# Optimization experiments

Measured on AMD Instinct MI355X. Metric: run time of the kernel, lower is better.

Reference implementation:

```python
import jax, jax.numpy as jnp
import numpy as np

B, S, D = 4, 2048, 1024
H = 16
HS = D // H  # 64


def setup_inputs() -> dict:
    key = jax.random.key(0)
    ks = jax.random.split(key, 6)
    scale = 1.0 / np.sqrt(D)
    x = jax.random.normal(ks[0], (B, S, D), dtype=jnp.float32)
    # per-head projection weights, stacked: [H, D, HS]
    Wq = jax.random.normal(ks[1], (H, D, HS), dtype=jnp.float32) * scale
    Wk = jax.random.normal(ks[2], (H, D, HS), dtype=jnp.float32) * scale
    Wv = jax.random.normal(ks[3], (H, D, HS), dtype=jnp.float32) * scale
    Wo = jax.random.normal(ks[4], (D, D), dtype=jnp.float32) * scale
    bo = jax.random.normal(ks[5], (D,), dtype=jnp.float32) * 0.01
    return {"x": x, "Wq": Wq, "Wk": Wk, "Wv": Wv, "Wo": Wo, "bo": bo}


def reference(x, Wq, Wk, Wv, Wo, bo):
    # Per-head dense projections (no bias): [B,S,D] x [H,D,HS] -> [B,H,S,HS]
    q = jnp.einsum('bsd,hde->bhse', x, Wq)
    k = jnp.einsum('bsd,hde->bhse', x, Wk)
    v = jnp.einsum('bsd,hde->bhse', x, Wv)
    # scaled dot-product scores: [B,H,S,S]
    scores = jnp.einsum('bhse,bhte->bhst', q, k) / jnp.sqrt(jnp.asarray(HS, dtype=x.dtype))
    # causal mask (lower triangular kept)
    causal = jnp.tril(jnp.ones((S, S), dtype=bool))
    scores = jnp.where(causal, scores, -jnp.inf)
    attn = jax.nn.softmax(scores, axis=-1)
    # dropout is identity at inference (rate handled as 0)
    out = jnp.einsum('bhst,bhte->bhse', attn, v)  # [B,H,S,HS]
    # concat heads: [B,S,H*HS] = [B,S,D]
    out = jnp.transpose(out, (0, 2, 1, 3)).reshape(B, S, D)
    return out @ Wo + bo
```

## Files before the change

### kernel.cpp

```cpp
#include <hip/hip_runtime.h>
#include <hip/hip_bf16.h>
#include <stdint.h>

#define NB 4
#define NS 2048
#define ND 1024
#define NH 16
#define NHS 64
#define NEG_BIG (-1e30f)
#define Q_SCALE 0.18033688011112042f

typedef __bf16 bf16x8 __attribute__((ext_vector_type(8)));
typedef float floatx4 __attribute__((ext_vector_type(4)));
typedef short s16x4 __attribute__((ext_vector_type(4)));

#if defined(__has_builtin)
#if __has_builtin(__builtin_amdgcn_mfma_f32_16x16x16bf16_1k)
#define HAVE_MFMA1K 1
#endif
#endif
#ifndef HAVE_MFMA1K
#define HAVE_MFMA1K 0
#endif

static constexpr size_t WSLAB = (size_t)NH * ND * NHS;
static constexpr size_t QSLAB = (size_t)NB * NH * NS * NHS;
static constexpr size_t XSLAB = (size_t)NB * NS * ND;

__device__ __forceinline__ uint16_t f2b(float f) {
    union { __hip_bfloat16 h; uint16_t u; } cv;
    cv.h = __float2bfloat16(f);
    return cv.u;
}

__device__ __forceinline__ void gll16(const void* g, void* l) {
  __builtin_amdgcn_global_load_lds(
      (__attribute__((address_space(1))) void*)(uintptr_t)g,
      (__attribute__((address_space(3))) void*)(uintptr_t)l,
      16, 0, 0);
}

__global__ __launch_bounds__(256) void k_prep(
    const float* __restrict__ x, const float* __restrict__ Wq,
    const float* __restrict__ Wk, const float* __restrict__ Wv,
    const float* __restrict__ Wo, uint16_t* __restrict__ xb,
    uint16_t* __restrict__ wt) {
  __shared__ __align__(16) uint16_t T[64][72];
  int bid = blockIdx.x;
  int tid = threadIdx.x;
  if (bid < 4096) {
    size_t i0 = ((size_t)bid * 256 + tid) * 8;
    float4 f0 = *(const float4*)&x[i0];
    float4 f1 = *(const float4*)&x[i0 + 4];
    __align__(16) uint16_t tmp[8];
    tmp[0] = f2b(f0.x); tmp[1] = f2b(f0.y); tmp[2] = f2b(f0.z); tmp[3] = f2b(f0.w);
    tmp[4] = f2b(f1.x); tmp[5] = f2b(f1.y); tmp[6] = f2b(f1.z); tmp[7] = f2b(f1.w);
    *(uint4*)&xb[i0] = *(uint4*)tmp;
    return;
  }
  bid -= 4096;
  const float* src; uint16_t* dst;
  int srcStride, dstStride, r0, c0;
  if (bid < 768) {
    int mat = bid >> 8;
    int rem = bid & 255;
    int h = rem >> 4, dt = rem & 15;
    const float* W = (mat == 0) ? Wq : (mat == 1) ? Wk : Wv;
    src = W + (size_t)h * (ND * NHS);
    dst = wt + (size_t)mat * WSLAB + (size_t)h * (NHS * ND);
    srcStride = NHS; dstStride = ND;
    r0 = dt * 64; c0 = 0;
  } else {
    int rem = bid - 768;
    int dt = rem >> 4, et = rem & 15;
    src = Wo; dst = wt + 3 * WSLAB;
    srcStride = ND; dstStride = ND;
    r0 = dt * 64; c0 = et * 64;
  }
  for (int u = tid; u < 1024; u += 256) {
    int row = u >> 4, cq = u & 15;
    float4 f = *(const float4*)&src[(size_t)(r0 + row) * srcStride + c0 + cq * 4];
    uint16_t* p = &T[row][cq * 4];
    p[0] = f2b(f.x); p[1] = f2b(f.y); p[2] = f2b(f.z); p[3] = f2b(f.w);
  }
  __syncthreads();
  for (int u = tid; u < 512; u += 256) {
    int c = u >> 3, cg = u & 7;
    __align__(16) uint16_t tmp[8];
    for (int j = 0; j < 8; j++) tmp[j] = T[cg * 8 + j][c];
    *(uint4*)&dst[(size_t)(c0 + c) * dstStride + r0 + cg * 8] = *(uint4*)tmp;
  }
}

__global__ __launch_bounds__(512, 2) void k_qkv(
    const uint16_t* __restrict__ xb, const uint16_t* __restrict__ wt,
    uint16_t* __restrict__ qkv) {
  __shared__ __align__(16) uint16_t L[8 * 8192];

  int bid = blockIdx.x;
  int swz = (bid & 7) * 48 + (bid >> 3);
  int m0 = (swz & 31) * 256;
  int n0 = (swz >> 5) * 256;

  int tid = threadIdx.x;
  int wave = tid >> 6, lane = tid & 63, quad = lane >> 4, l16 = lane & 15;
  int wr = wave >> 2, wc = wave & 3;

  const uint16_t* pA = xb + (size_t)(m0 + (tid >> 2)) * ND + (tid & 3) * 8;
  const uint16_t* pB = wt + (size_t)(n0 + (tid >> 2)) * ND + (tid & 3) * 8;
  const int ldsStageOff = wave * 512;

  const int offA = (wr * 128 + l16) * 32 + quad * 8;
  const int offB = (wc * 64 + l16) * 32 + quad * 8;

  floatx4 acc[8][4];
  #pragma unroll
  for (int i = 0; i < 8; i++)
    #pragma unroll
    for (int j = 0; j < 4; j++) acc[i][j] = (floatx4){0.f, 0.f, 0.f, 0.f};

#define STAGE(H)                                                                \
  do {                                                                          \
    int h_ = (H);                                                               \
    if (h_ < 64) {                                                              \
      const uint16_t* g_ = ((h_ & 1) ? pB : pA) + (h_ >> 2) * 64 + ((h_ >> 1) & 1) * 32; \
      uint16_t* l_ = &L[(h_ & 7) * 8192 + ldsStageOff];                         \
      gll16(g_, l_);                                                            \
      gll16(g_ + 128 * ND, l_ + 4096);                                          \
    }                                                                           \
  } while (0)

#define PH_BAR()                         \
  do {                                   \
    asm volatile("" ::: "memory");       \
    __builtin_amdgcn_s_barrier();        \
    asm volatile("" ::: "memory");       \
  } while (0)

  STAGE(0); STAGE(1); STAGE(2); STAGE(3); STAGE(4); STAGE(5);
  asm volatile("s_waitcnt vmcnt(4)" ::: "memory");
  PH_BAR();

  bf16x8 bfr[4];

#define MFMA16(QM)                                                                                   \
  acc[(QM)*4+0][0] = __builtin_amdgcn_mfma_f32_16x16x32_bf16(af0_, bfr[0], acc[(QM)*4+0][0],0,0,0);  \
  acc[(QM)*4+0][1] = __builtin_amdgcn_mfma_f32_16x16x32_bf16(af0_, bfr[1], acc[(QM)*4+0][1],0,0,0);  \
  acc[(QM)*4+0][2] = __builtin_amdgcn_mfma_f32_16x16x32_bf16(af0_, bfr[2], acc[(QM)*4+0][2],0,0,0);  \
  acc[(QM)*4+0][3] = __builtin_amdgcn_mfma_f32_16x16x32_bf16(af0_, bfr[3], acc[(QM)*4+0][3],0,0,0);  \
  acc[(QM)*4+1][0] = __builtin_amdgcn_mfma_f32_16x16x32_bf16(af1_, bfr[0], acc[(QM)*4+1][0],0,0,0);  \
  acc[(QM)*4+1][1] = __builtin_amdgcn_mfma_f32_16x16x32_bf16(af1_, bfr[1], acc[(QM)*4+1][1],0,0,0);  \
  acc[(QM)*4+1][2] = __builtin_amdgcn_mfma_f32_16x16x32_bf16(af1_, bfr[2], acc[(QM)*4+1][2],0,0,0);  \
  acc[(QM)*4+1][3] = __builtin_amdgcn_mfma_f32_16x16x32_bf16(af1_, bfr[3], acc[(QM)*4+1][3],0,0,0);  \
  acc[(QM)*4+2][0] = __builtin_amdgcn_mfma_f32_16x16x32_bf16(af2_, bfr[0], acc[(QM)*4+2][0],0,0,0);  \
  acc[(QM)*4+2][1] = __builtin_amdgcn_mfma_f32_16x16x32_bf16(af2_, bfr[1], acc[(QM)*4+2][1],0,0,0);  \
  acc[(QM)*4+2][2] = __builtin_amdgcn_mfma_f32_16x16x32_bf16(af2_, bfr[2], acc[(QM)*4+2][2],0,0,0);  \
  acc[(QM)*4+2][3] = __builtin_amdgcn_mfma_f32_16x16x32_bf16(af2_, bfr[3], acc[(QM)*4+2][3],0,0,0);  \
  acc[(QM)*4+3][0] = __builtin_amdgcn_mfma_f32_16x16x32_bf16(af3_, bfr[0], acc[(QM)*4+3][0],0,0,0);  \
  acc[(QM)*4+3][1] = __builtin_amdgcn_mfma_f32_16x16x32_bf16(af3_, bfr[1], acc[(QM)*4+3][1],0,0,0);  \
  acc[(QM)*4+3][2] = __builtin_amdgcn_mfma_f32_16x16x32_bf16(af3_, bfr[2], acc[(QM)*4+3][2],0,0,0);  \
  acc[(QM)*4+3][3] = __builtin_amdgcn_mfma_f32_16x16x32_bf16(af3_, bfr[3], acc[(QM)*4+3][3],0,0,0)

#define PHASE(T4, KK, QM, HSTAGE, LOADB)                                        \
  {                                                                             \
    const int slA_ = (((T4) + 2 * (KK)) & 7) * 8192;                            \
    bf16x8 af0_ = *(const bf16x8*)&L[slA_ + offA + (QM) * 2048 + 0 * 512];      \
    bf16x8 af1_ = *(const bf16x8*)&L[slA_ + offA + (QM) * 2048 + 1 * 512];      \
    bf16x8 af2_ = *(const bf16x8*)&L[slA_ + offA + (QM) * 2048 + 2 * 512];      \
    bf16x8 af3_ = *(const bf16x8*)&L[slA_ + offA + (QM) * 2048 + 3 * 512];      \
    if (LOADB) {                                                                \
      const int slB_ = (((T4) + 2 * (KK) + 1) & 7) * 8192;                      \
      bfr[0] = *(const bf16x8*)&L[slB_ + offB + 0 * 512];                       \
      bfr[1] = *(const bf16x8*)&L[slB_ + offB + 1 * 512];                       \
      bfr[2] = *(const bf16x8*)&L[slB_ + offB + 2 * 512];                       \
      bfr[3] = *(const bf16x8*)&L[slB_ + offB + 3 * 512];                       \
    }                                                                           \
    STAGE(HSTAGE);                                                              \
    PH_BAR();                                                                   \
    __builtin_amdgcn_s_setprio(1);                                              \
    MFMA16(QM);                                                                 \
    __builtin_amdgcn_s_setprio(0);                                              \
  }

  for (int t = 0; t < 16; ++t) {
    int t4 = t * 4;
    PHASE(t4, 0, 0, t4 + 6, 1);
    PH_BAR();
    PHASE(t4, 0, 1, t4 + 7, 0);
    PH_BAR();
    PHASE(t4, 1, 0, t4 + 8, 1);
    PH_BAR();
    PHASE(t4, 1, 1, t4 + 9, 0);
    if (t < 14)       { asm volatile("s_waitcnt vmcnt(4)" ::: "memory"); }
    else if (t == 14) { asm volatile("s_waitcnt vmcnt(0)" ::: "memory"); }
    PH_BAR();
  }
#undef PHASE
#undef MFMA16
#undef STAGE
#undef PH_BAR

  int matid = n0 >> 10;
  float scale = (matid == 0) ? Q_SCALE : 1.0f;
  uint16_t* base = qkv + (size_t)matid * QSLAB;
  int hh = ((n0 & 1023) >> 6) + wc;
  #pragma unroll
  for (int mq = 0; mq < 8; mq++) {
    int m = m0 + wr * 128 + mq * 16 + quad * 4;
    int b = m >> 11, s = m & 2047;
    size_t rbase = ((size_t)(b * 16 + hh) * NS + s) * NHS;
    #pragma unroll
    for (int nt = 0; nt < 4; nt++)
      #pragma unroll
      for (int r = 0; r < 4; r++)
        base[rbase + (size_t)r * NHS + nt * 16 + l16] = f2b(acc[mq][nt][r] * scale);
  }
}

__global__ __launch_bounds__(256) void k_vt(
    const uint16_t* __restrict__ v, uint16_t* __restrict__ vt) {
  __shared__ __align__(16) uint16_t T[64][72];
  int bh = blockIdx.y;
  int s0 = blockIdx.x * 64;
  int tid = threadIdx.x;
  const uint16_t* src = v + (size_t)bh * (NS * NHS);
  uint16_t* dst = vt + (size_t)bh * (NS * NHS);
  for (int u = tid; u < 512; u += 256) {
    int row = u >> 3, cg = u & 7;
    *(uint4*)&T[row][cg * 8] =
        *(const uint4*)&src[(size_t)(s0 + row) * NHS + cg * 8];
  }
  __syncthreads();
  for (int u = tid; u < 512; u += 256) {
    int e = u >> 3, cg = u & 7;
    __align__(16) uint16_t tmp[8];
    for (int j = 0; j < 8; j++) tmp[j] = T[cg * 8 + j][e];
    *(uint4*)&dst[(size_t)e * NS + s0 + cg * 8] = *(uint4*)tmp;
  }
}

#if HAVE_MFMA1K
__global__ __launch_bounds__(256, 4) void k_attn(
    const uint16_t* __restrict__ Q, const uint16_t* __restrict__ K,
    const uint16_t* __restrict__ VT, uint16_t* __restrict__ Y) {
  __shared__ __align__(16) uint16_t Ks[64][72];
  __shared__ __align__(16) uint16_t Vs[64][72];
  int bh = blockIdx.y;
  int b = bh >> 4, h = bh & 15;
  int ta = blockIdx.x;
  int tb = 31 - ta;
  const uint16_t* Qp = Q + (size_t)bh * (NS * NHS);
  const uint16_t* Kp = K + (size_t)bh * (NS * NHS);
  const uint16_t* Vp = VT + (size_t)bh * (NS * NHS);
  int tid = threadIdx.x;
  int wv = tid >> 6, lane = tid & 63, quad = lane >> 4, l16 = lane & 15;

  int row0 = tid >> 3, cg0 = tid & 7;
  int row1 = (tid + 256) >> 3, cg1 = tid & 7;

  int rA = ta * 64 + wv * 16 + l16;
  int rB = tb * 64 + wv * 16 + l16;
  bf16x8 aqA0 = *(const bf16x8*)&Qp[(size_t)rA * NHS + quad * 8];
  bf16x8 aqA1 = *(const bf16x8*)&Qp[(size_t)rA * NHS + 32 + quad * 8];
  bf16x8 aqB0 = *(const bf16x8*)&Qp[(size_t)rB * NHS + quad * 8];
  bf16x8 aqB1 = *(const bf16x8*)&Qp[(size_t)rB * NHS + 32 + quad * 8];

  float lAs = 0.f, lBs = 0.f;
  floatx4 oA[4], oB[4];
  for (int et = 0; et < 4; et++) {
    oA[et] = (floatx4){0.f, 0.f, 0.f, 0.f};
    oB[et] = (floatx4){0.f, 0.f, 0.f, 0.f};
  }

  uint4 rk0, rk1, rv0, rv1;
  rk0 = *(const uint4*)&Kp[(size_t)(0 * 64 + row0) * NHS + cg0 * 8];
  rk1 = *(const uint4*)&Kp[(size_t)(0 * 64 + row1) * NHS + cg1 * 8];
  rv0 = *(const uint4*)&Vp[(size_t)row0 * NS + 0 * 64 + cg0 * 8];
  rv1 = *(const uint4*)&Vp[(size_t)row1 * NS + 0 * 64 + cg1 * 8];

  for (int kt = 0; kt <= tb; kt++) {
    bool doA = (kt <= ta);
    __syncthreads();
    *(uint4*)&Ks[row0][cg0 * 8] = rk0;
    *(uint4*)&Ks[row1][cg1 * 8] = rk1;
    *(uint4*)&Vs[row0][cg0 * 8] = rv0;
    *(uint4*)&Vs[row1][cg1 * 8] = rv1;
    __syncthreads();
    if (kt < tb) {
      rk0 = *(const uint4*)&Kp[(size_t)((kt + 1) * 64 + row0) * NHS + cg0 * 8];
      rk1 = *(const uint4*)&Kp[(size_t)((kt + 1) * 64 + row1) * NHS + cg1 * 8];
      rv0 = *(const uint4*)&Vp[(size_t)row0 * NS + (kt + 1) * 64 + cg0 * 8];
      rv1 = *(const uint4*)&Vp[(size_t)row1 * NS + (kt + 1) * 64 + cg1 * 8];
    }

    s16x4 pbA[4], pbB[4];
    for (int ct = 0; ct < 4; ct++) {
      bf16x8 kb0 = *(const bf16x8*)&Ks[ct * 16 + l16][quad * 8];
      bf16x8 kb1 = *(const bf16x8*)&Ks[ct * 16 + l16][32 + quad * 8];
      int key = kt * 64 + ct * 16 + quad * 4;
      floatx4 c = (floatx4){0.f, 0.f, 0.f, 0.f};
      c = __builtin_amdgcn_mfma_f32_16x16x32_bf16(kb0, aqB0, c, 0, 0, 0);
      c = __builtin_amdgcn_mfma_f32_16x16x32_bf16(kb1, aqB1, c, 0, 0, 0);
      for (int r = 0; r < 4; r++) {
        float s = (kt == tb && key + r > rB) ? NEG_BIG : c[r];
        float p = __builtin_amdgcn_exp2f(s);
        lBs += p;
        pbB[ct][r] = (short)f2b(p);
      }
      if (doA) {
        floatx4 d = (floatx4){0.f, 0.f, 0.f, 0.f};
        d = __builtin_amdgcn_mfma_f32_16x16x32_bf16(kb0, aqA0, d, 0, 0, 0);
        d = __builtin_amdgcn_mfma_f32_16x16x32_bf16(kb1, aqA1, d, 0, 0, 0);
        for (int r = 0; r < 4; r++) {
          float s = (kt == ta && key + r > rA) ? NEG_BIG : d[r];
          float p = __builtin_amdgcn_exp2f(s);
          lAs += p;
          pbA[ct][r] = (short)f2b(p);
        }
      }
    }
    for (int et = 0; et < 4; et++)
      for (int ct = 0; ct < 4; ct++) {
        s16x4 va = *(const s16x4*)&Vs[et * 16 + l16][ct * 16 + quad * 4];
        oB[et] = __builtin_amdgcn_mfma_f32_16x16x16bf16_1k(va, pbB[ct], oB[et], 0, 0, 0);
        if (doA)
          oA[et] = __builtin_amdgcn_mfma_f32_16x16x16bf16_1k(va, pbA[ct], oA[et], 0, 0, 0);
      }
  }
  lAs += __shfl_xor(lAs, 16, 64); lAs += __shfl_xor(lAs, 32, 64);
  lBs += __shfl_xor(lBs, 16, 64); lBs += __shfl_xor(lBs, 32, 64);
  float invA = 1.f / lAs, invB = 1.f / lBs;
  uint16_t* yb = Y + (size_t)b * NS * ND + (size_t)h * NHS;
  for (int et = 0; et < 4; et++) {
    __align__(8) uint16_t tA[4], tB[4];
    for (int r = 0; r < 4; r++) {
      tA[r] = f2b(oA[et][r] * invA);
      tB[r] = f2b(oB[et][r] * invB);
    }
    *(uint2*)&yb[(size_t)rA * ND + et * 16 + quad * 4] = *(uint2*)tA;
    *(uint2*)&yb[(size_t)rB * ND + et * 16 + quad * 4] = *(uint2*)tB;
  }
}
#else
__global__ __launch_bounds__(256) void k_attn(
    const uint16_t* __restrict__ Q, const uint16_t* __restrict__ K,
    const uint16_t* __restrict__ VT, uint16_t* __restrict__ Y) {
  __shared__ __align__(16) uint16_t Ks[64][72];
  __shared__ __align__(16) uint16_t Vs[64][72];
  __shared__ __align__(16) uint16_t Ps[4][2][16][72];
  int bh = blockIdx.y;
  int b = bh >> 4, h = bh & 15;
  int ta = blockIdx.x;
  int tb = 31 - ta;
  const uint16_t* Qp = Q + (size_t)bh * (NS * NHS);
  const uint16_t* Kp = K + (size_t)bh * (NS * NHS);
  const uint16_t* Vp = VT + (size_t)bh * (NS * NHS);
  int tid = threadIdx.x;
  int wv = tid >> 6, lane = tid & 63, quad = lane >> 4, l16 = lane & 15;

  int rA = ta * 64 + wv * 16 + l16;
  int rB = tb * 64 + wv * 16 + l16;
  bf16x8 aqA0 = *(const bf16x8*)&Qp[(size_t)rA * NHS + quad * 8];
  bf16x8 aqA1 = *(const bf16x8*)&Qp[(size_t)rA * NHS + 32 + quad * 8];
  bf16x8 aqB0 = *(const bf16x8*)&Qp[(size_t)rB * NHS + quad * 8];
  bf16x8 aqB1 = *(const bf16x8*)&Qp[(size_t)rB * NHS + 32 + quad * 8];

  float lA[4] = {0.f, 0.f, 0.f, 0.f}, lB[4] = {0.f, 0.f, 0.f, 0.f};
  floatx4 oA[4], oB[4];
  for (int ct = 0; ct < 4; ct++) {
    oA[ct] = (floatx4){0.f, 0.f, 0.f, 0.f};
    oB[ct] = (floatx4){0.f, 0.f, 0.f, 0.f};
  }
  for (int kt = 0; kt <= tb; kt++) {
    bool doA = (kt <= ta);
    __syncthreads();
    for (int u = tid; u < 512; u += 256) {
      int row = u >> 3, cg = u & 7;
      *(uint4*)&Ks[row][cg * 8] =
          *(const uint4*)&Kp[(size_t)(kt * 64 + row) * NHS + cg * 8];
    }
    for (int u = tid; u < 512; u += 256) {
      int row = u >> 3, cg = u & 7;
      *(uint4*)&Vs[row][cg * 8] =
          *(const uint4*)&Vp[(size_t)row * NS + kt * 64 + cg * 8];
    }
    __syncthreads();
    floatx4 sA[4], sB[4];
    for (int ct = 0; ct < 4; ct++) {
      bf16x8 kb0 = *(const bf16x8*)&Ks[ct * 16 + l16][quad * 8];
      bf16x8 kb1 = *(const bf16x8*)&Ks[ct * 16 + l16][32 + quad * 8];
      floatx4 c = (floatx4){0.f, 0.f, 0.f, 0.f};
      c = __builtin_amdgcn_mfma_f32_16x16x32_bf16(aqB0, kb0, c, 0, 0, 0);
      c = __builtin_amdgcn_mfma_f32_16x16x32_bf16(aqB1, kb1, c, 0, 0, 0);
      sB[ct] = c;
      if (doA) {
        floatx4 d = (floatx4){0.f, 0.f, 0.f, 0.f};
        d = __builtin_amdgcn_mfma_f32_16x16x32_bf16(aqA0, kb0, d, 0, 0, 0);
        d = __builtin_amdgcn_mfma_f32_16x16x32_bf16(aqA1, kb1, d, 0, 0, 0);
        sA[ct] = d;
      }
    }
    if (kt == tb) {
      int qrb = tb * 64 + wv * 16 + quad * 4;
      for (int ct = 0; ct < 4; ct++) {
        int kg = kt * 64 + ct * 16 + l16;
        for (int r = 0; r < 4; r++)
          sB[ct][r] = (kg <= qrb + r) ? sB[ct][r] : NEG_BIG;
      }
    }
    if (doA && kt == ta) {
      int qrb = ta * 64 + wv * 16 + quad * 4;
      for (int ct = 0; ct < 4; ct++) {
        int kg = kt * 64 + ct * 16 + l16;
        for (int r = 0; r < 4; r++)
          sA[ct][r] = (kg <= qrb + r) ? sA[ct][r] : NEG_BIG;
      }
    }
    for (int ct = 0; ct < 4; ct++)
      for (int r = 0; r < 4; r++) {
        float p = __builtin_amdgcn_exp2f(sB[ct][r]);
        lB[r] += p;
        Ps[wv][1][quad * 4 + r][ct * 16 + l16] = f2b(p);
      }
    if (doA)
      for (int ct = 0; ct < 4; ct++)
        for (int r = 0; r < 4; r++) {
          float p = __builtin_amdgcn_exp2f(sA[ct][r]);
          lA[r] += p;
          Ps[wv][0][quad * 4 + r][ct * 16 + l16] = f2b(p);
        }
    bf16x8 apB0 = *(const bf16x8*)&Ps[wv][1][l16][quad * 8];
    bf16x8 apB1 = *(const bf16x8*)&Ps[wv][1][l16][32 + quad * 8];
    bf16x8 apA0, apA1;
    if (doA) {
      apA0 = *(const bf16x8*)&Ps[wv][0][l16][quad * 8];
      apA1 = *(const bf16x8*)&Ps[wv][0][l16][32 + quad * 8];
    }
    for (int ct = 0; ct < 4; ct++) {
      bf16x8 vb0 = *(const bf16x8*)&Vs[ct * 16 + l16][quad * 8];
      bf16x8 vb1 = *(const bf16x8*)&Vs[ct * 16 + l16][32 + quad * 8];
      oB[ct] = __builtin_amdgcn_mfma_f32_16x16x32_bf16(apB0, vb0, oB[ct], 0, 0, 0);
      oB[ct] = __builtin_amdgcn_mfma_f32_16x16x32_bf16(apB1, vb1, oB[ct], 0, 0, 0);
      if (doA) {
        oA[ct] = __builtin_amdgcn_mfma_f32_16x16x32_bf16(apA0, vb0, oA[ct], 0, 0, 0);
        oA[ct] = __builtin_amdgcn_mfma_f32_16x16x32_bf16(apA1, vb1, oA[ct], 0, 0, 0);
      }
    }
  }
  for (int off = 1; off < 16; off <<= 1)
    for (int r = 0; r < 4; r++) {
      lA[r] += __shfl_xor(lA[r], off, 64);
      lB[r] += __shfl_xor(lB[r], off, 64);
    }
  uint16_t* yb = Y + (size_t)b * NS * ND + (size_t)h * NHS;
  for (int ct = 0; ct < 4; ct++)
    for (int r = 0; r < 4; r++) {
      int sA_ = ta * 64 + wv * 16 + quad * 4 + r;
      int sB_ = tb * 64 + wv * 16 + quad * 4 + r;
      yb[(size_t)sA_ * ND + ct * 16 + l16] = f2b(oA[ct][r] / lA[r]);
      yb[(size_t)sB_ * ND + ct * 16 + l16] = f2b(oB[ct][r] / lB[r]);
    }
}
#endif

__global__ __launch_bounds__(256) void k_proj(
    const uint16_t* __restrict__ y, const uint16_t* __restrict__ wot,
    const float* __restrict__ bo, float* __restrict__ out) {
  __shared__ __align__(16) uint16_t As[128 * 64];
  __shared__ __align__(16) uint16_t Bs[128 * 64];
  int m0 = blockIdx.x * 128;
  int n0 = blockIdx.y * 128;
  int tid = threadIdx.x;
  int wv = tid >> 6, lane = tid & 63, quad = lane >> 4, l16 = lane & 15;
  int wr = wv >> 1, wc = wv & 1;
  int srow = lane >> 3, scol = lane & 7;

  floatx4 acc[4][4];
  for (int i = 0; i < 4; i++)
    for (int j = 0; j < 4; j++) acc[i][j] = (floatx4){0.f, 0.f, 0.f, 0.f};

  for (int k0 = 0; k0 < ND; k0 += 64) {
    __syncthreads();
    for (int j = 0; j < 4; j++) {
      int rg = wv * 4 + j;
      int r = rg * 8 + srow;
      gll16(&y[(size_t)(m0 + r) * ND + k0 + scol * 8], &As[rg * 512]);
      gll16(&wot[(size_t)(n0 + r) * ND + k0 + scol * 8], &Bs[rg * 512]);
    }
    __syncthreads();
    for (int kk = 0; kk < 2; kk++) {
      bf16x8 af[4], bfr[4];
      for (int t = 0; t < 4; t++) {
        af[t]  = *(const bf16x8*)&As[(wr * 64 + t * 16 + l16) * 64 + kk * 32 + quad * 8];
        bfr[t] = *(const bf16x8*)&Bs[(wc * 64 + t * 16 + l16) * 64 + kk * 32 + quad * 8];
      }
      for (int mt = 0; mt < 4; mt++)
        for (int nt = 0; nt < 4; nt++)
          acc[mt][nt] = __builtin_amdgcn_mfma_f32_16x16x32_bf16(af[mt], bfr[nt], acc[mt][nt], 0, 0, 0);
    }
  }
  for (int mt = 0; mt < 4; mt++)
    for (int nt = 0; nt < 4; nt++)
      for (int r = 0; r < 4; r++) {
        int s = m0 + wr * 64 + mt * 16 + quad * 4 + r;
        int n = n0 + wc * 64 + nt * 16 + l16;
        out[(size_t)s * ND + n] = acc[mt][nt][r] + bo[n];
      }
}

extern "C" void kernel_launch(void* const* d_in, const int* in_sizes, int n_in,
                              void* d_out, int out_size, void* d_ws, size_t ws_size,
                              hipStream_t stream) {
  const float* x  = (const float*)d_in[0];
  const float* Wq = (const float*)d_in[1];
  const float* Wk = (const float*)d_in[2];
  const float* Wv = (const float*)d_in[3];
  const float* Wo = (const float*)d_in[4];
  const float* bo = (const float*)d_in[5];
  uint16_t* ws = (uint16_t*)d_ws;

  uint16_t* wt = ws;
  uint16_t* xb = ws + 4 * WSLAB;
  uint16_t* q  = xb + XSLAB;
  uint16_t* k  = q + QSLAB;
  uint16_t* v  = k + QSLAB;
  uint16_t* y  = v + QSLAB;
  uint16_t* vt = y + QSLAB;

  k_prep<<<dim3(5120), dim3(256), 0, stream>>>(x, Wq, Wk, Wv, Wo, xb, wt);
  k_qkv<<<dim3(384), dim3(512), 0, stream>>>(xb, wt, q);
  k_vt<<<dim3(NS / 64, NB * NH), dim3(256), 0, stream>>>(v, vt);
  k_attn<<<dim3(16, NB * NH), dim3(256), 0, stream>>>(q, k, vt, y);
  k_proj<<<dim3(64, 8), dim3(256), 0, stream>>>(y, wt + 3 * WSLAB, bo, (float*)d_out);
}
```

Before: 268.9 us.

## Fuse V transpose into QKV GEMM epilogue via LDS staging

The QKV projection kernel now writes V directly in transposed layout: blocks computing the V slab stage their accumulators in padded LDS and emit coalesced 16-byte stores into the VT buffer. This removes the separate k_vt launch and its round trip of V through global memory. The block-to-tile swizzle is also changed so each XCD handles a contiguous group of M tiles, and the LDS stage stride is padded to 8704 to fit the transpose buffer, which raises LDS use per block.

After: 263.5 us. -2.0%, faster.

```diff
diff --git a/kernel.cpp b/kernel.cpp
--- a/kernel.cpp
+++ b/kernel.cpp
@@ -94,13 +94,15 @@
 
 __global__ __launch_bounds__(512, 2) void k_qkv(
     const uint16_t* __restrict__ xb, const uint16_t* __restrict__ wt,
-    uint16_t* __restrict__ qkv) {
-  __shared__ __align__(16) uint16_t L[8 * 8192];
+    uint16_t* __restrict__ qk, uint16_t* __restrict__ vt) {
+  __shared__ __align__(16) uint16_t L[8 * 8704];
 
   int bid = blockIdx.x;
-  int swz = (bid & 7) * 48 + (bid >> 3);
-  int m0 = (swz & 31) * 256;
-  int n0 = (swz >> 5) * 256;
+  int xcd = bid & 7, idx = bid >> 3;
+  int mt = xcd * 4 + (idx & 3);
+  int ntile = idx >> 2;
+  int m0 = mt * 256;
+  int n0 = ntile * 256;
 
   int tid = threadIdx.x;
   int wave = tid >> 6, lane = tid & 63, quad = lane >> 4, l16 = lane & 15;
@@ -124,7 +126,7 @@
     int h_ = (H);                                                               \
     if (h_ < 64) {                                                              \
       const uint16_t* g_ = ((h_ & 1) ? pB : pA) + (h_ >> 2) * 64 + ((h_ >> 1) & 1) * 32; \
-      uint16_t* l_ = &L[(h_ & 7) * 8192 + ldsStageOff];                         \
+      uint16_t* l_ = &L[(h_ & 7) * 8704 + ldsStageOff];                         \
       gll16(g_, l_);                                                            \
       gll16(g_ + 128 * ND, l_ + 4096);                                          \
     }                                                                           \
@@ -163,13 +165,13 @@
 
 #define PHASE(T4, KK, QM, HSTAGE, LOADB)                                        \
   {                                                                             \
-    const int slA_ = (((T4) + 2 * (KK)) & 7) * 8192;                            \
+    const int slA_ = (((T4) + 2 * (KK)) & 7) * 8704;                            \
     bf16x8 af0_ = *(const bf16x8*)&L[slA_ + offA + (QM) * 2048 + 0 * 512];      \
     bf16x8 af1_ = *(const bf16x8*)&L[slA_ + offA + (QM) * 2048 + 1 * 512];      \
     bf16x8 af2_ = *(const bf16x8*)&L[slA_ + offA + (QM) * 2048 + 2 * 512];      \
     bf16x8 af3_ = *(const bf16x8*)&L[slA_ + offA + (QM) * 2048 + 3 * 512];      \
     if (LOADB) {                                                                \
-      const int slB_ = (((T4) + 2 * (KK) + 1) & 7) * 8192;                      \
+      const int slB_ = (((T4) + 2 * (KK) + 1) & 7) * 8704;                      \
       bfr[0] = *(const bf16x8*)&L[slB_ + offB + 0 * 512];                       \
       bfr[1] = *(const bf16x8*)&L[slB_ + offB + 1 * 512];                       \
       bfr[2] = *(const bf16x8*)&L[slB_ + offB + 2 * 512];                       \
@@ -201,41 +203,45 @@
 #undef PH_BAR
 
   int matid = n0 >> 10;
-  float scale = (matid == 0) ? Q_SCALE : 1.0f;
-  uint16_t* base = qkv + (size_t)matid * QSLAB;
-  int hh = ((n0 & 1023) >> 6) + wc;
-  #pragma unroll
-  for (int mq = 0; mq < 8; mq++) {
-    int m = m0 + wr * 128 + mq * 16 + quad * 4;
-    int b = m >> 11, s = m & 2047;
-    size_t rbase = ((size_t)(b * 16 + hh) * NS + s) * NHS;
+  if (matid == 2) {
+    uint16_t* wbuf = &L[wave * 8704];
     #pragma unroll
-    for (int nt = 0; nt < 4; nt++)
+    for (int mq = 0; mq < 8; mq++)
       #pragma unroll
-      for (int r = 0; r < 4; r++)
-        base[rbase + (size_t)r * NHS + nt * 16 + l16] = f2b(acc[mq][nt][r] * scale);
-  }
-}
-
-__global__ __launch_bounds__(256) void k_vt(
-    const uint16_t* __restrict__ v, uint16_t* __restrict__ vt) {
-  __shared__ __align__(16) uint16_t T[64][72];
-  int bh = blockIdx.y;
-  int s0 = blockIdx.x * 64;
-  int tid = threadIdx.x;
-  const uint16_t* src = v + (size_t)bh * (NS * NHS);
-  uint16_t* dst = vt + (size_t)bh * (NS * NHS);
-  for (int u = tid; u < 512; u += 256) {
-    int row = u >> 3, cg = u & 7;
-    *(uint4*)&T[row][cg * 8] =
-        *(const uint4*)&src[(size_t)(s0 + row) * NHS + cg * 8];
-  }
-  __syncthreads();
-  for (int u = tid; u < 512; u += 256) {
-    int e = u >> 3, cg = u & 7;
-    __align__(16) uint16_t tmp[8];
-    for (int j = 0; j < 8; j++) tmp[j] = T[cg * 8 + j][e];
-    *(uint4*)&dst[(size_t)e * NS + s0 + cg * 8] = *(uint4*)tmp;
+      for (int nt = 0; nt < 4; nt++) {
+        __align__(8) uint16_t t4v[4];
+        #pragma unroll
+        for (int r = 0; r < 4; r++) t4v[r] = f2b(acc[mq][nt][r]);
+        int e = nt * 16 + l16;
+        *(uint2*)&wbuf[e * 136 + mq * 16 + quad * 4] = *(uint2*)t4v;
+      }
+    __syncthreads();
+    int hb = (n0 - 2048) >> 6;
+    int b = m0 >> 11, s0m = m0 & 2047;
+    #pragma unroll
+    for (int i = 0; i < 16; i++) {
+      int c = i * 512 + tid;
+      int row = c >> 5, sb = c & 31;
+      int hl = row >> 6, e = row & 63;
+      int wsrc = (sb >> 4) * 4 + hl;
+      uint4 d = *(const uint4*)&L[wsrc * 8704 + e * 136 + (sb & 15) * 8];
+      *(uint4*)&vt[((size_t)(b * 16 + hb + hl) * 64 + e) * 2048 + s0m + sb * 8] = d;
+    }
+  } else {
+    float scale = (matid == 0) ? Q_SCALE : 1.0f;
+    uint16_t* base = qk + (size_t)matid * QSLAB;
+    int hh = ((n0 & 1023) >> 6) + wc;
+    #pragma unroll
+    for (int mq = 0; mq < 8; mq++) {
+      int m = m0 + wr * 128 + mq * 16 + quad * 4;
+      int b = m >> 11, s = m & 2047;
+      size_t rbase = ((size_t)(b * 16 + hh) * NS + s) * NHS;
+      #pragma unroll
+      for (int nt = 0; nt < 4; nt++)
+        #pragma unroll
+        for (int r = 0; r < 4; r++)
+          base[rbase + (size_t)r * NHS + nt * 16 + l16] = f2b(acc[mq][nt][r] * scale);
+    }
   }
 }
 
@@ -523,13 +529,11 @@
   uint16_t* xb = ws + 4 * WSLAB;
   uint16_t* q  = xb + XSLAB;
   uint16_t* k  = q + QSLAB;
-  uint16_t* v  = k + QSLAB;
-  uint16_t* y  = v + QSLAB;
-  uint16_t* vt = y + QSLAB;
+  uint16_t* vt = k + QSLAB;
+  uint16_t* y  = vt + QSLAB;
 
   k_prep<<<dim3(5120), dim3(256), 0, stream>>>(x, Wq, Wk, Wv, Wo, xb, wt);
-  k_qkv<<<dim3(384), dim3(512), 0, stream>>>(xb, wt, q);
-  k_vt<<<dim3(NS / 64, NB * NH), dim3(256), 0, stream>>>(v, vt);
+  k_qkv<<<dim3(384), dim3(512), 0, stream>>>(xb, wt, q, vt);
   k_attn<<<dim3(16, NB * NH), dim3(256), 0, stream>>>(q, k, vt, y);
   k_proj<<<dim3(64, 8), dim3(256), 0, stream>>>(y, wt + 3 * WSLAB, bo, (float*)d_out);
 }
```
